# Kernel tuning notes

Hardware: AMD Instinct MI355X
Metric: run time of the kernel (lower is better)

The kernel has to match this reference:

```python
import jax, jax.numpy as jnp
import numpy as np

N_HEADS = 16
D_MODEL = 512
HEAD_DIM = D_MODEL // N_HEADS
SCALE = 1.0 / (HEAD_DIM ** 0.5)
R = 4  # LSREF radius -> window = step = 2*r = 8


def _layernorm(x, g, b, eps=1e-5):
    m = x.mean(axis=-1, keepdims=True)
    v = x.var(axis=-1, keepdims=True)
    return (x - m) / jnp.sqrt(v + eps) * g + b


def _mha(q_in, k_in, v_in, wq, bq, wk, bk, wv, bv, wo, bo):
    # Informer FullAttention(mask_flag=False), AttentionLayer(mix=False), eval mode (no dropout)
    B, L, _ = q_in.shape
    S = k_in.shape[1]
    q = (q_in @ wq.T + bq).reshape(B, L, N_HEADS, HEAD_DIM)
    k = (k_in @ wk.T + bk).reshape(B, S, N_HEADS, HEAD_DIM)
    v = (v_in @ wv.T + bv).reshape(B, S, N_HEADS, HEAD_DIM)
    scores = jnp.einsum('blhe,bshe->bhls', q, k) * SCALE
    A = jax.nn.softmax(scores, axis=-1)
    out = jnp.einsum('bhls,bshd->blhd', A, v).reshape(B, L, D_MODEL)
    return out @ wo.T + bo


def setup_inputs() -> dict:
    key = jax.random.key(0)
    ks = jax.random.split(key, 32)
    B, L, C, GL, DFF = 4, 1024, 512, 4096, 2048

    def w(k, shape, s=0.02):
        return (jax.random.normal(k, shape, jnp.float32) * s).astype(jnp.float32)

    inp = {
        'x': jax.random.normal(ks[0], (B, L, C), jnp.float32),
        'global_feat': jax.random.normal(ks[1], (B, C, GL), jnp.float32),
        'conv_w': w(ks[2], (C, C)), 'conv_b': jnp.zeros((C,), jnp.float32),
        'sa_wq': w(ks[3], (C, C)), 'sa_bq': jnp.zeros((C,), jnp.float32),
        'sa_wk': w(ks[4], (C, C)), 'sa_bk': jnp.zeros((C,), jnp.float32),
        'sa_wv': w(ks[5], (C, C)), 'sa_bv': jnp.zeros((C,), jnp.float32),
        'sa_wo': w(ks[6], (C, C)), 'sa_bo': jnp.zeros((C,), jnp.float32),
        'ca_wq': w(ks[7], (C, C)), 'ca_bq': jnp.zeros((C,), jnp.float32),
        'ca_wk': w(ks[8], (C, C)), 'ca_bk': jnp.zeros((C,), jnp.float32),
        'ca_wv': w(ks[9], (C, C)), 'ca_bv': jnp.zeros((C,), jnp.float32),
        'ca_wo': w(ks[10], (C, C)), 'ca_bo': jnp.zeros((C,), jnp.float32),
        'ffn_w1': w(ks[11], (DFF, C)), 'ffn_b1': jnp.zeros((DFF,), jnp.float32),
        'ffn_w2': w(ks[12], (C, DFF)), 'ffn_b2': jnp.zeros((C,), jnp.float32),
        'n1_g': jnp.ones((C,), jnp.float32), 'n1_b': jnp.zeros((C,), jnp.float32),
        'n2_g': jnp.ones((C,), jnp.float32), 'n2_b': jnp.zeros((C,), jnp.float32),
        'n3_g': jnp.ones((C,), jnp.float32), 'n3_b': jnp.zeros((C,), jnp.float32),
    }
    return inp


def reference(x, global_feat, conv_w, conv_b,
              sa_wq, sa_bq, sa_wk, sa_bk, sa_wv, sa_bv, sa_wo, sa_bo,
              ca_wq, ca_bq, ca_wk, ca_bk, ca_wv, ca_bv, ca_wo, ca_bo,
              ffn_w1, ffn_b1, ffn_w2, ffn_b2,
              n1_g, n1_b, n2_g, n2_b, n3_g, n3_b):
    # --- sliding_window_gaussian: non-overlapping windows (step == window == 2r) ---
    B, C, GL = global_feat.shape
    win_sz = 2 * R
    nw = (GL - win_sz) // win_sz + 1
    win = global_feat[:, :, :nw * win_sz].reshape(B, C, nw, win_sz)
    # torch.norm over a keepdim=1 axis is just |max - min|
    res = jnp.abs(win.max(axis=-1) - win.min(axis=-1)) + 1e-6  # [B, C, nw]
    # conv1d kernel size 1 == channelwise linear, then relu
    res = jax.nn.relu(jnp.einsum('oc,bcn->bon', conv_w, res) + conv_b[None, :, None])
    cross = res  # [B, 512, nw=512] consumed as [B, S, d_model]

    # --- CrossPyramidFusion: one Informer-style layer (self-attn, cross-attn, conv FFN) ---
    h = x + _mha(x, x, x, sa_wq, sa_bq, sa_wk, sa_bk, sa_wv, sa_bv, sa_wo, sa_bo)
    h = _layernorm(h, n1_g, n1_b)
    h = h + _mha(h, cross, cross, ca_wq, ca_bq, ca_wk, ca_bk, ca_wv, ca_bv, ca_wo, ca_bo)
    h = _layernorm(h, n2_g, n2_b)
    y = jax.nn.gelu(h @ ffn_w1.T + ffn_b1, approximate=False)
    y = y @ ffn_w2.T + ffn_b2
    out = _layernorm(h + y, n3_g, n3_b)
    return out.transpose(0, 2, 1)  # [B, 512, L]
```

## Files before the change

kernel.cpp:

```cpp
#include <hip/hip_runtime.h>
#include <hip/hip_bf16.h>
#include <math.h>

#define SCALE_Q 0.25504522f

typedef unsigned short u16;
typedef unsigned int u32;
typedef __attribute__((ext_vector_type(8))) short bshort8;
typedef __attribute__((ext_vector_type(4))) short sshort4;
typedef __attribute__((ext_vector_type(4))) float f32x4;
typedef __attribute__((ext_vector_type(4))) u32 u32x4;

__device__ inline u16 f2b(float f) {
    union { float f; uint32_t u; } c;
    c.f = f;
    uint32_t u = c.u;
    return (u16)((u + 0x7fffu + ((u >> 16) & 1u)) >> 16);
}

__device__ __forceinline__ u32 cvtpk(float a, float b) {
    u32 r;
    asm("v_cvt_pk_bf16_f32 %0, %1, %2" : "=v"(r) : "v"(a), "v"(b));
    return r;
}

__device__ __forceinline__ float exp2c(float s) {
    float c = fminf(s, 100.f);
    float r;
    asm("v_exp_f32 %0, %1" : "=v"(r) : "v"(c));
    return r;
}

__device__ inline void gload_lds16(const void* g, void* lds) {
    __builtin_amdgcn_global_load_lds(
        (const __attribute__((address_space(1))) void*)g,
        (__attribute__((address_space(3))) void*)lds, 16, 0, 0);
}

struct WSrc { const float* p[12]; };
__global__ __launch_bounds__(256) void wconv_kernel(WSrc s, u16* __restrict__ dst) {
    long e = ((long)blockIdx.x * 256 + threadIdx.x) * 4;
    if (e >= 6553600) return;
    int w; long base;
    if (e < 2359296)      { w = (int)(e >> 18); base = (long)w << 18; }
    else if (e < 3407872) { w = 9;  base = 2359296; }
    else if (e < 4456448) { w = 10; base = 3407872; }
    else                  { w = 11; base = 4456448; }
    float4 v = *(const float4*)(s.p[w] + (e - base));
    dst[e + 0] = f2b(v.x); dst[e + 1] = f2b(v.y);
    dst[e + 2] = f2b(v.z); dst[e + 3] = f2b(v.w);
}

__global__ __launch_bounds__(256) void win_kernel(const float* __restrict__ G,
                                                  u16* __restrict__ Rt, int total) {
    int i = blockIdx.x * 256 + threadIdx.x;
    if (i >= total) return;
    const float4* p = reinterpret_cast<const float4*>(G) + (size_t)i * 2;
    float4 a = p[0], b = p[1];
    float mx = fmaxf(fmaxf(fmaxf(a.x, a.y), fmaxf(a.z, a.w)),
                     fmaxf(fmaxf(b.x, b.y), fmaxf(b.z, b.w)));
    float mn = fminf(fminf(fminf(a.x, a.y), fminf(a.z, a.w)),
                     fminf(fminf(b.x, b.y), fminf(b.z, b.w)));
    int b_ = i >> 18, c = (i >> 9) & 511, n = i & 511;
    Rt[((long)(b_ * 512 + n) << 9) + c] = f2b(fabsf(mx - mn) + 1e-6f);
}

template <int BIASMODE, int ACT, bool RESID, int OUTMODE>
__device__ __forceinline__ void gemm_epilogue_elem(
    float v, int row, int col, int N, long zoff,
    const float* bias, const float* Rres, void* Cout,
    u16* D1, u16* D2, const float* bias1, const float* bias2) {
    if (OUTMODE == 3) {
        int grp = col >> 9, c = col & 511;
        float bb = (grp == 0) ? bias[c] : (grp == 1) ? bias1[c] : bias2[c];
        float vv = v + bb;
        if (grp == 0)
            ((u16*)Cout)[(long)row * 512 + c] = f2b(vv * SCALE_Q);
        else if (grp == 1)
            D1[(long)row * 512 + c] = f2b(vv);
        else
            D2[((long)((row >> 10) * 512 + c) << 10) + (row & 1023)] = f2b(vv);
    } else if (OUTMODE == 4) {
        int grp = col >> 9, c = col & 511;
        float vv = v + ((grp == 0) ? bias[c] : bias1[c]);
        if (grp == 0)
            ((u16*)Cout)[(long)row * 512 + c] = f2b(vv);
        else
            D2[((long)((row >> 9) * 512 + c) << 9) + (row & 511)] = f2b(vv);
    } else {
        if (BIASMODE == 1) v += bias[col];
        if (BIASMODE == 2) v += bias[row];
        if (ACT == 1) v = fmaxf(v, 0.f);
        if (ACT == 2) v = 0.5f * v * (1.f + erff(v * 0.70710678118654752f));
        if (ACT == 3) v *= SCALE_Q;
        if (RESID) v += Rres[(long)row * N + col];
        long off = zoff + (long)row * N + col;
        if (OUTMODE == 1) ((u16*)Cout)[off] = f2b(v);
        else              ((float*)Cout)[off] = v;
    }
}

template <int BIASMODE, int ACT, bool RESID, int OUTMODE>
__global__ __launch_bounds__(256) void bgemm64_kernel(
    const u16* __restrict__ A, const u16* __restrict__ Bt,
    const float* __restrict__ bias, const float* __restrict__ Rres,
    void* __restrict__ Cout, int M, int N, int K,
    long sA, long sB, long sC,
    u16* __restrict__ D1, u16* __restrict__ D2,
    const float* __restrict__ bias1, const float* __restrict__ bias2) {
    A  += (long)blockIdx.z * sA;
    Bt += (long)blockIdx.z * sB;
    __shared__ u16 As[2][64 * 64];
    __shared__ u16 Bs[2][64 * 64];
    int tid = threadIdx.x;
    int lane = tid & 63, wv = tid >> 6;
    int wr = wv >> 1, wc = wv & 1;
    int m0 = blockIdx.x * 64, n0 = blockIdx.y * 64;
    f32x4 acc[2][2] = {};
    int srow = lane >> 3;
    int selem = ((lane & 7) ^ srow) << 3;

    auto STAGE = [&](int buf, int k0) {
        #pragma unroll
        for (int i = 0; i < 2; i++) {
            int roff = i * 32 + wv * 8;
            gload_lds16(A + (long)(m0 + roff + srow) * K + k0 + selem,
                        (char*)As[buf] + roff * 128);
            gload_lds16(Bt + (long)(n0 + roff + srow) * K + k0 + selem,
                        (char*)Bs[buf] + roff * 128);
        }
    };

    int NT = K >> 6;
    STAGE(0, 0);
    int cur = 0;
    for (int kt = 0; kt < NT; ++kt) {
        if (kt + 1 < NT) {
            STAGE(cur ^ 1, (kt + 1) << 6);
            asm volatile("s_waitcnt vmcnt(4)\ns_barrier" ::: "memory");
        } else {
            asm volatile("s_waitcnt vmcnt(0)\ns_barrier" ::: "memory");
        }
        #pragma unroll
        for (int ks = 0; ks < 2; ks++) {
            bshort8 af[2], bf[2];
            int kbo = ks * 64 + ((lane >> 4) << 4);
            #pragma unroll
            for (int f = 0; f < 2; f++) {
                int arow = wr * 32 + f * 16 + (lane & 15);
                af[f] = *(const bshort8*)((const char*)As[cur] + arow * 128 +
                                          (kbo ^ ((arow & 7) << 4)));
                int brow = wc * 32 + f * 16 + (lane & 15);
                bf[f] = *(const bshort8*)((const char*)Bs[cur] + brow * 128 +
                                          (kbo ^ ((brow & 7) << 4)));
            }
            #pragma unroll
            for (int fi = 0; fi < 2; fi++)
                #pragma unroll
                for (int fj = 0; fj < 2; fj++)
                    acc[fi][fj] = __builtin_amdgcn_mfma_f32_16x16x32_bf16(
                        af[fi], bf[fj], acc[fi][fj], 0, 0, 0);
        }
        asm volatile("s_barrier" ::: "memory");
        cur ^= 1;
    }
    long zoff = (long)blockIdx.z * sC;
    #pragma unroll
    for (int fi = 0; fi < 2; fi++)
        #pragma unroll
        for (int fj = 0; fj < 2; fj++)
            #pragma unroll
            for (int r = 0; r < 4; r++) {
                int row = m0 + wr * 32 + fi * 16 + ((lane >> 4) << 2) + r;
                int col = n0 + wc * 32 + fj * 16 + (lane & 15);
                gemm_epilogue_elem<BIASMODE, ACT, RESID, OUTMODE>(
                    acc[fi][fj][r], row, col, N, zoff, bias, Rres, Cout,
                    D1, D2, bias1, bias2);
            }
}

__global__ __launch_bounds__(512) void attn_mfma_kernel(
    const u16* __restrict__ Q, const u16* __restrict__ K,
    const u16* __restrict__ Vt, u16* __restrict__ O, int L, int S) {
    __shared__ __align__(16) u16 Ks[2][2048];
    __shared__ __align__(16) u16 Vs[2][2048];
    int bh = blockIdx.x;
    int b = bh >> 4, h = bh & 15;
    int tid = threadIdx.x;
    int lane = tid & 63, wv = tid >> 6;
    int q0 = blockIdx.y * 128 + wv * 16;
    int qr = lane & 15, g = lane >> 4, g8 = g * 8;
    int kperm = 8 * (qr >> 2) + (qr & 3);
    int nt = S >> 6;

    const u16* Kb = K + (long)b * S * 512 + h * 32;
    const u16* Vb = Vt + ((long)b * 512 + h * 32) * S;
    bshort8 qf = *(const bshort8*)(Q + ((long)(b * L + q0 + qr)) * 512 + h * 32 + g8);

    const u16* src;
    long step;
    char *d0, *d1;
    if (wv < 4) {
        int rk = wv * 16 + (lane >> 2);
        int f = ((rk >> 3) & 3) ^ ((rk >> 1) & 3);
        int sc = (lane & 3) ^ f;
        src = Kb + (long)rk * 512 + sc * 8;
        step = (long)64 * 512;
        d0 = (char*)Ks[0] + wv * 1024;
        d1 = (char*)Ks[1] + wv * 1024;
    } else {
        int rv = (wv - 4) * 8 + (lane >> 3);
        int sc = (lane & 7) ^ (lane >> 3);
        src = Vb + (long)rv * S + sc * 8;
        step = 64;
        d0 = (char*)Vs[0] + (wv - 4) * 1024;
        d1 = (char*)Vs[1] + (wv - 4) * 1024;
    }

    f32x4 acc0 = {}, acc1 = {};
    float lsum = 0.f;
    int f0 = (qr >> 2) ^ ((qr >> 1) & 1);
    int f1 = f0 ^ 2;

    gload_lds16(src, d0);
    int cur = 0;
    for (int t = 0; t < nt; ++t) {
        if (t + 1 < nt) {
            gload_lds16(src + (long)(t + 1) * step, cur ? d0 : d1);
            asm volatile("s_waitcnt vmcnt(1)\ns_barrier" ::: "memory");
        } else {
            asm volatile("s_waitcnt vmcnt(0)\ns_barrier" ::: "memory");
        }
        const char* Kt = (const char*)Ks[cur];
        const char* Vl = (const char*)Vs[cur];
        bshort8 a0 = *(const bshort8*)(Kt + kperm * 64 + ((g ^ f0) << 4));
        bshort8 a1 = *(const bshort8*)(Kt + (kperm + 4) * 64 + ((g ^ f1) << 4));
        bshort8 a2 = *(const bshort8*)(Kt + (kperm + 32) * 64 + ((g ^ f0) << 4));
        bshort8 a3 = *(const bshort8*)(Kt + (kperm + 36) * 64 + ((g ^ f1) << 4));
        bshort8 v00 = *(const bshort8*)(Vl + qr * 128 + ((g ^ (qr & 7)) << 4));
        bshort8 v01 = *(const bshort8*)(Vl + qr * 128 + (((g + 4) ^ (qr & 7)) << 4));
        bshort8 v10 = *(const bshort8*)(Vl + (16 + qr) * 128 + ((g ^ (qr & 7)) << 4));
        bshort8 v11 = *(const bshort8*)(Vl + (16 + qr) * 128 + (((g + 4) ^ (qr & 7)) << 4));
        f32x4 zz = {0.f, 0.f, 0.f, 0.f};
        f32x4 st0 = __builtin_amdgcn_mfma_f32_16x16x32_bf16(a0, qf, zz, 0, 0, 0);
        f32x4 st1 = __builtin_amdgcn_mfma_f32_16x16x32_bf16(a1, qf, zz, 0, 0, 0);
        f32x4 st2 = __builtin_amdgcn_mfma_f32_16x16x32_bf16(a2, qf, zz, 0, 0, 0);
        f32x4 st3 = __builtin_amdgcn_mfma_f32_16x16x32_bf16(a3, qf, zz, 0, 0, 0);
        float p0[4], p1[4], p2[4], p3[4];
        #pragma unroll
        for (int r = 0; r < 4; r++) {
            p0[r] = exp2c(st0[r]);
            p1[r] = exp2c(st1[r]);
            p2[r] = exp2c(st2[r]);
            p3[r] = exp2c(st3[r]);
        }
        float ps = ((p0[0] + p0[1]) + (p0[2] + p0[3])) + ((p1[0] + p1[1]) + (p1[2] + p1[3])) +
                   ((p2[0] + p2[1]) + (p2[2] + p2[3])) + ((p3[0] + p3[1]) + (p3[2] + p3[3]));
        lsum += ps;
        u32x4 P0 = { cvtpk(p0[0], p0[1]), cvtpk(p0[2], p0[3]),
                     cvtpk(p1[0], p1[1]), cvtpk(p1[2], p1[3]) };
        u32x4 P1 = { cvtpk(p2[0], p2[1]), cvtpk(p2[2], p2[3]),
                     cvtpk(p3[0], p3[1]), cvtpk(p3[2], p3[3]) };
        bshort8 pf0 = *(bshort8*)&P0;
        bshort8 pf1 = *(bshort8*)&P1;
        acc0 = __builtin_amdgcn_mfma_f32_16x16x32_bf16(v00, pf0, acc0, 0, 0, 0);
        acc0 = __builtin_amdgcn_mfma_f32_16x16x32_bf16(v01, pf1, acc0, 0, 0, 0);
        acc1 = __builtin_amdgcn_mfma_f32_16x16x32_bf16(v10, pf0, acc1, 0, 0, 0);
        acc1 = __builtin_amdgcn_mfma_f32_16x16x32_bf16(v11, pf1, acc1, 0, 0, 0);
        asm volatile("s_barrier" ::: "memory");
        cur ^= 1;
    }

    lsum += __shfl_xor(lsum, 16);
    lsum += __shfl_xor(lsum, 32);
    float inv = 1.f / lsum;
    u16* op = O + ((long)(b * L + q0 + qr)) * 512 + h * 32 + g * 4;
    sshort4 o0, o1;
    #pragma unroll
    for (int r = 0; r < 4; r++) {
        o0[r] = (short)f2b(acc0[r] * inv);
        o1[r] = (short)f2b(acc1[r] * inv);
    }
    *(sshort4*)op = o0;
    *(sshort4*)(op + 16) = o1;
}

__global__ __launch_bounds__(256) void ln_kernel(const float* __restrict__ X,
                                                 const float* __restrict__ g,
                                                 const float* __restrict__ bt,
                                                 float* __restrict__ Y,
                                                 u16* __restrict__ Yb) {
    int row = blockIdx.x;
    const float* xr = X + (long)row * 512;
    int t = threadIdx.x;
    float x0 = xr[t], x1 = xr[t + 256];
    float s = x0 + x1, ss = x0 * x0 + x1 * x1;
    #pragma unroll
    for (int off = 32; off > 0; off >>= 1) {
        s += __shfl_down(s, off);
        ss += __shfl_down(ss, off);
    }
    __shared__ float sred[4], ssred[4];
    int wid = t >> 6;
    if ((t & 63) == 0) { sred[wid] = s; ssred[wid] = ss; }
    __syncthreads();
    float ts = sred[0] + sred[1] + sred[2] + sred[3];
    float tss = ssred[0] + ssred[1] + ssred[2] + ssred[3];
    float mean = ts * (1.f / 512.f);
    float var = tss * (1.f / 512.f) - mean * mean;
    float rstd = rsqrtf(var + 1e-5f);
    float y0 = (x0 - mean) * rstd * g[t] + bt[t];
    float y1 = (x1 - mean) * rstd * g[t + 256] + bt[t + 256];
    Y[(long)row * 512 + t] = y0;
    Y[(long)row * 512 + t + 256] = y1;
    Yb[(long)row * 512 + t] = f2b(y0);
    Yb[(long)row * 512 + t + 256] = f2b(y1);
}

__global__ __launch_bounds__(256) void ln_stats_kernel(const float* __restrict__ X,
                                                       float2* __restrict__ stats) {
    int row = blockIdx.x * 4 + (threadIdx.x >> 6);
    int lane = threadIdx.x & 63;
    const float4* xr = (const float4*)(X + (long)row * 512) + lane * 2;
    float4 a = xr[0], b = xr[1];
    float s = (a.x + a.y) + (a.z + a.w) + (b.x + b.y) + (b.z + b.w);
    float ss = (a.x * a.x + a.y * a.y) + (a.z * a.z + a.w * a.w) +
               (b.x * b.x + b.y * b.y) + (b.z * b.z + b.w * b.w);
    #pragma unroll
    for (int off = 32; off > 0; off >>= 1) {
        s += __shfl_down(s, off);
        ss += __shfl_down(ss, off);
    }
    if (lane == 0) {
        float mean = s * (1.f / 512.f);
        float var = ss * (1.f / 512.f) - mean * mean;
        stats[row] = make_float2(mean, rsqrtf(var + 1e-5f));
    }
}

__global__ __launch_bounds__(256) void ln_trans_kernel(
    const float* __restrict__ X, const float2* __restrict__ stats,
    const float* __restrict__ g, const float* __restrict__ bt,
    float* __restrict__ Y) {
    __shared__ float T[64][65];
    int b = blockIdx.z, l0 = blockIdx.x * 64, c0 = blockIdx.y * 64;
    int t = threadIdx.x;
    int col = t & 63, rq = t >> 6;
    #pragma unroll
    for (int i = 0; i < 16; i++) {
        int row = i * 4 + rq;
        T[row][col] = X[((long)(b * 1024 + l0 + row)) * 512 + c0 + col];
    }
    __syncthreads();
    float2 mr = stats[b * 1024 + l0 + col];
    #pragma unroll
    for (int i = 0; i < 16; i++) {
        int c = i * 4 + rq;
        float val = (T[col][c] - mr.x) * mr.y * g[c0 + c] + bt[c0 + c];
        Y[((long)(b * 512 + c0 + c)) * 1024 + l0 + col] = val;
    }
}

extern "C" void kernel_launch(void* const* d_in, const int* in_sizes, int n_in,
                              void* d_out, int out_size, void* d_ws, size_t ws_size,
                              hipStream_t stream) {
    const float* x      = (const float*)d_in[0];
    const float* gfeat  = (const float*)d_in[1];
    const float* conv_w = (const float*)d_in[2];
    const float* conv_b = (const float*)d_in[3];
    const float* sa_wq = (const float*)d_in[4];
    const float* sa_bq = (const float*)d_in[5];
    const float* sa_wk = (const float*)d_in[6];
    const float* sa_bk = (const float*)d_in[7];
    const float* sa_wv = (const float*)d_in[8];
    const float* sa_bv = (const float*)d_in[9];
    const float* sa_wo = (const float*)d_in[10];
    const float* sa_bo = (const float*)d_in[11];
    const float* ca_wq = (const float*)d_in[12];
    const float* ca_bq = (const float*)d_in[13];
    const float* ca_wk = (const float*)d_in[14];
    const float* ca_bk = (const float*)d_in[15];
    const float* ca_wv = (const float*)d_in[16];
    const float* ca_bv = (const float*)d_in[17];
    const float* ca_wo = (const float*)d_in[18];
    const float* ca_bo = (const float*)d_in[19];
    const float* ffn_w1 = (const float*)d_in[20];
    const float* ffn_b1 = (const float*)d_in[21];
    const float* ffn_w2 = (const float*)d_in[22];
    const float* ffn_b2 = (const float*)d_in[23];
    const float* n1_g = (const float*)d_in[24];
    const float* n1_b = (const float*)d_in[25];
    const float* n2_g = (const float*)d_in[26];
    const float* n2_b = (const float*)d_in[27];
    const float* n3_g = (const float*)d_in[28];
    const float* n3_b = (const float*)d_in[29];
    (void)ws_size; (void)n_in; (void)in_sizes; (void)out_size;

    const long M_ = 1048576;
    float* W0 = (float*)d_ws;
    float* h   = W0;
    float* hn  = W0 + 2 * M_;
    u16* U = (u16*)(W0 + 4 * M_);
    u16* qb     = U;
    u16* kb     = U + 2 * M_;
    u16* vtb    = U + 4 * M_;
    u16* k2b    = U + 6 * M_;
    u16* v2tb   = U + 7 * M_;
    u16* attb   = U + 8 * M_;
    u16* hnb    = U + 10 * M_;
    u16* midb   = U + 12 * M_;
    u16* wsb    = U + 20 * M_;
    u16* res_tb = U + 27 * M_;
    u16* crossb = U + 28 * M_;

    float2* ln3_stats = (float2*)res_tb;

    const u16* conv_wb = wsb;
    const u16* sa_wqb = wsb + 262144;
    const u16* sa_wob = wsb + 1048576;
    const u16* ca_wqb = wsb + 1310720;
    const u16* ca_wkb = wsb + 1572864;
    const u16* ca_wob = wsb + 2097152;
    const u16* ffn1b = wsb + 2359296, *ffn2b = wsb + 3407872;
    const u16* xb = wsb + 4456448;

    WSrc ws;
    ws.p[0] = conv_w; ws.p[1] = sa_wq; ws.p[2] = sa_wk; ws.p[3] = sa_wv;
    ws.p[4] = sa_wo; ws.p[5] = ca_wq; ws.p[6] = ca_wk; ws.p[7] = ca_wv;
    ws.p[8] = ca_wo; ws.p[9] = ffn_w1; ws.p[10] = ffn_w2; ws.p[11] = x;
    wconv_kernel<<<6400, 256, 0, stream>>>(ws, wsb);

    win_kernel<<<4096, 256, 0, stream>>>(gfeat, res_tb, 4 * 512 * 512);

    bgemm64_kernel<2, 1, false, 1><<<dim3(8, 8, 4), 256, 0, stream>>>(
        conv_wb, res_tb, conv_b, nullptr, crossb, 512, 512, 512, 0, 262144, 262144,
        nullptr, nullptr, nullptr, nullptr);

    bgemm64_kernel<1, 0, false, 3><<<dim3(64, 24), 256, 0, stream>>>(
        xb, sa_wqb, sa_bq, nullptr, qb, 4096, 1536, 512, 0, 0, 0,
        kb, vtb, sa_bk, sa_bv);

    attn_mfma_kernel<<<dim3(64, 8), 512, 0, stream>>>(qb, kb, vtb, attb, 1024, 1024);

    bgemm64_kernel<1, 0, true, 0><<<dim3(64, 8), 256, 0, stream>>>(
        attb, sa_wob, sa_bo, x, h, 4096, 512, 512, 0, 0, 0,
        nullptr, nullptr, nullptr, nullptr);

    ln_kernel<<<4096, 256, 0, stream>>>(h, n1_g, n1_b, hn, hnb);

    bgemm64_kernel<1, 3, false, 1><<<dim3(64, 8), 256, 0, stream>>>(
        hnb, ca_wqb, ca_bq, nullptr, qb, 4096, 512, 512, 0, 0, 0,
        nullptr, nullptr, nullptr, nullptr);
    bgemm64_kernel<1, 0, false, 4><<<dim3(32, 16), 256, 0, stream>>>(
        crossb, ca_wkb, ca_bk, nullptr, k2b, 2048, 1024, 512, 0, 0, 0,
        nullptr, v2tb, ca_bv, nullptr);

    attn_mfma_kernel<<<dim3(64, 8), 512, 0, stream>>>(qb, k2b, v2tb, attb, 1024, 512);

    bgemm64_kernel<1, 0, true, 0><<<dim3(64, 8), 256, 0, stream>>>(
        attb, ca_wob, ca_bo, hn, h, 4096, 512, 512, 0, 0, 0,
        nullptr, nullptr, nullptr, nullptr);

    ln_kernel<<<4096, 256, 0, stream>>>(h, n2_g, n2_b, hn, hnb);

    bgemm64_kernel<1, 2, false, 1><<<dim3(64, 32), 256, 0, stream>>>(
        hnb, ffn1b, ffn_b1, nullptr, midb, 4096, 2048, 512, 0, 0, 0,
        nullptr, nullptr, nullptr, nullptr);

    bgemm64_kernel<1, 0, true, 0><<<dim3(64, 8), 256, 0, stream>>>(
        midb, ffn2b, ffn_b2, hn, h, 4096, 512, 2048, 0, 0, 0,
        nullptr, nullptr, nullptr, nullptr);

    ln_stats_kernel<<<1024, 256, 0, stream>>>(h, ln3_stats);
    ln_trans_kernel<<<dim3(16, 8, 4), 256, 0, stream>>>(
        h, ln3_stats, n3_g, n3_b, (float*)d_out);
}
```

Baseline: 173.9 us.

## Merge prep kernels with LDS-transposed window reduce; triple-buffer attention loads

```diff
diff --git a/kernel.cpp b/kernel.cpp
--- a/kernel.cpp
+++ b/kernel.cpp
@@ -38,31 +38,44 @@
 }
 
 struct WSrc { const float* p[12]; };
-__global__ __launch_bounds__(256) void wconv_kernel(WSrc s, u16* __restrict__ dst) {
-    long e = ((long)blockIdx.x * 256 + threadIdx.x) * 4;
-    if (e >= 6553600) return;
-    int w; long base;
-    if (e < 2359296)      { w = (int)(e >> 18); base = (long)w << 18; }
-    else if (e < 3407872) { w = 9;  base = 2359296; }
-    else if (e < 4456448) { w = 10; base = 3407872; }
-    else                  { w = 11; base = 4456448; }
-    float4 v = *(const float4*)(s.p[w] + (e - base));
-    dst[e + 0] = f2b(v.x); dst[e + 1] = f2b(v.y);
-    dst[e + 2] = f2b(v.z); dst[e + 3] = f2b(v.w);
-}
-
-__global__ __launch_bounds__(256) void win_kernel(const float* __restrict__ G,
-                                                  u16* __restrict__ Rt, int total) {
-    int i = blockIdx.x * 256 + threadIdx.x;
-    if (i >= total) return;
-    const float4* p = reinterpret_cast<const float4*>(G) + (size_t)i * 2;
-    float4 a = p[0], b = p[1];
-    float mx = fmaxf(fmaxf(fmaxf(a.x, a.y), fmaxf(a.z, a.w)),
-                     fmaxf(fmaxf(b.x, b.y), fmaxf(b.z, b.w)));
-    float mn = fminf(fminf(fminf(a.x, a.y), fminf(a.z, a.w)),
-                     fminf(fminf(b.x, b.y), fminf(b.z, b.w)));
-    int b_ = i >> 18, c = (i >> 9) & 511, n = i & 511;
-    Rt[((long)(b_ * 512 + n) << 9) + c] = f2b(fabsf(mx - mn) + 1e-6f);
+__global__ __launch_bounds__(256) void prep_kernel(WSrc s, u16* __restrict__ dst,
+                                                   const float* __restrict__ G,
+                                                   u16* __restrict__ Rt) {
+    int bid = blockIdx.x;
+    if (bid < 256) {
+        __shared__ u16 T[64][72];
+        int b = bid >> 6, c0 = ((bid >> 3) & 7) << 6, n0 = (bid & 7) << 6;
+        int t = threadIdx.x;
+        int n = t & 63, cq = t >> 6;
+        const float* Gb = G + (long)b * 512 * 4096;
+        #pragma unroll
+        for (int i = 0; i < 16; i++) {
+            int c = i * 4 + cq;
+            const float4* p = (const float4*)(Gb + (long)(c0 + c) * 4096 + (n0 + n) * 8);
+            float4 a = p[0], bb = p[1];
+            float mx = fmaxf(fmaxf(fmaxf(a.x, a.y), fmaxf(a.z, a.w)),
+                             fmaxf(fmaxf(bb.x, bb.y), fmaxf(bb.z, bb.w)));
+            float mn = fminf(fminf(fminf(a.x, a.y), fminf(a.z, a.w)),
+                             fminf(fminf(bb.x, bb.y), fminf(bb.z, bb.w)));
+            T[n][c] = f2b(fabsf(mx - mn) + 1e-6f);
+        }
+        __syncthreads();
+        int nr = t >> 2, ck = (t & 3) << 4;
+        u16* o = Rt + ((long)(b * 512 + n0 + nr) << 9) + c0 + ck;
+        *(bshort8*)o = *(const bshort8*)&T[nr][ck];
+        *(bshort8*)(o + 8) = *(const bshort8*)&T[nr][ck + 8];
+    } else {
+        long e = ((long)(bid - 256) * 256 + threadIdx.x) * 4;
+        if (e >= 6553600) return;
+        int w; long base;
+        if (e < 2359296)      { w = (int)(e >> 18); base = (long)w << 18; }
+        else if (e < 3407872) { w = 9;  base = 2359296; }
+        else if (e < 4456448) { w = 10; base = 3407872; }
+        else                  { w = 11; base = 4456448; }
+        float4 v = *(const float4*)(s.p[w] + (e - base));
+        dst[e + 0] = f2b(v.x); dst[e + 1] = f2b(v.y);
+        dst[e + 2] = f2b(v.z); dst[e + 3] = f2b(v.w);
+    }
 }
 
 template <int BIASMODE, int ACT, bool RESID, int OUTMODE>
@@ -182,8 +195,8 @@
 __global__ __launch_bounds__(512) void attn_mfma_kernel(
     const u16* __restrict__ Q, const u16* __restrict__ K,
     const u16* __restrict__ Vt, u16* __restrict__ O, int L, int S) {
-    __shared__ __align__(16) u16 Ks[2][2048];
-    __shared__ __align__(16) u16 Vs[2][2048];
+    __shared__ __align__(16) u16 Ks[3][2048];
+    __shared__ __align__(16) u16 Vs[3][2048];
     int bh = blockIdx.x;
     int b = bh >> 4, h = bh & 15;
     int tid = threadIdx.x;
@@ -199,7 +212,7 @@
 
     const u16* src;
     long step;
-    char *d0, *d1;
+    char* d0;
     if (wv < 4) {
         int rk = wv * 16 + (lane >> 2);
         int f = ((rk >> 3) & 3) ^ ((rk >> 1) & 3);
@@ -207,32 +220,35 @@
         src = Kb + (long)rk * 512 + sc * 8;
         step = (long)64 * 512;
         d0 = (char*)Ks[0] + wv * 1024;
-        d1 = (char*)Ks[1] + wv * 1024;
     } else {
         int rv = (wv - 4) * 8 + (lane >> 3);
         int sc = (lane & 7) ^ (lane >> 3);
         src = Vb + (long)rv * S + sc * 8;
         step = 64;
         d0 = (char*)Vs[0] + (wv - 4) * 1024;
-        d1 = (char*)Vs[1] + (wv - 4) * 1024;
-    }
-
-    f32x4 acc0 = {}, acc1 = {};
-    float lsum = 0.f;
+    }
+
+    f32x4 acc0 = {}, acc1 = {}, acc2 = {};
+    const bshort8 onesf = { (short)0x3F80, (short)0x3F80, (short)0x3F80, (short)0x3F80,
+                            (short)0x3F80, (short)0x3F80, (short)0x3F80, (short)0x3F80 };
     int f0 = (qr >> 2) ^ ((qr >> 1) & 1);
     int f1 = f0 ^ 2;
 
     gload_lds16(src, d0);
+    gload_lds16(src + step, d0 + 4096);
     int cur = 0;
     for (int t = 0; t < nt; ++t) {
-        if (t + 1 < nt) {
-            gload_lds16(src + (long)(t + 1) * step, cur ? d0 : d1);
+        if (t + 2 < nt) {
+            int nb = cur + 2; if (nb >= 3) nb -= 3;
+            gload_lds16(src + (long)(t + 2) * step, d0 + nb * 4096);
+            asm volatile("s_waitcnt vmcnt(2)\ns_barrier" ::: "memory");
+        } else if (t + 1 < nt) {
             asm volatile("s_waitcnt vmcnt(1)\ns_barrier" ::: "memory");
         } else {
             asm volatile("s_waitcnt vmcnt(0)\ns_barrier" ::: "memory");
         }
-        const char* Kt = (const char*)Ks[cur];
-        const char* Vl = (const char*)Vs[cur];
+        const char* Kt = (const char*)Ks[0] + cur * 4096;
+        const char* Vl = (const char*)Vs[0] + cur * 4096;
         bshort8 a0 = *(const bshort8*)(Kt + kperm * 64 + ((g ^ f0) << 4));
         bshort8 a1 = *(const bshort8*)(Kt + (kperm + 4) * 64 + ((g ^ f1) << 4));
         bshort8 a2 = *(const bshort8*)(Kt + (kperm + 32) * 64 + ((g ^ f0) << 4));
@@ -254,9 +270,6 @@
             p2[r] = exp2c(st2[r]);
             p3[r] = exp2c(st3[r]);
         }
-        float ps = ((p0[0] + p0[1]) + (p0[2] + p0[3])) + ((p1[0] + p1[1]) + (p1[2] + p1[3])) +
-                   ((p2[0] + p2[1]) + (p2[2] + p2[3])) + ((p3[0] + p3[1]) + (p3[2] + p3[3]));
-        lsum += ps;
         u32x4 P0 = { cvtpk(p0[0], p0[1]), cvtpk(p0[2], p0[3]),
                      cvtpk(p1[0], p1[1]), cvtpk(p1[2], p1[3]) };
         u32x4 P1 = { cvtpk(p2[0], p2[1]), cvtpk(p2[2], p2[3]),
@@ -267,13 +280,13 @@
         acc0 = __builtin_amdgcn_mfma_f32_16x16x32_bf16(v01, pf1, acc0, 0, 0, 0);
         acc1 = __builtin_amdgcn_mfma_f32_16x16x32_bf16(v10, pf0, acc1, 0, 0, 0);
         acc1 = __builtin_amdgcn_mfma_f32_16x16x32_bf16(v11, pf1, acc1, 0, 0, 0);
+        acc2 = __builtin_amdgcn_mfma_f32_16x16x32_bf16(onesf, pf0, acc2, 0, 0, 0);
+        acc2 = __builtin_amdgcn_mfma_f32_16x16x32_bf16(onesf, pf1, acc2, 0, 0, 0);
         asm volatile("s_barrier" ::: "memory");
-        cur ^= 1;
-    }
-
-    lsum += __shfl_xor(lsum, 16);
-    lsum += __shfl_xor(lsum, 32);
-    float inv = 1.f / lsum;
+        cur = (cur == 2) ? 0 : cur + 1;
+    }
+
+    float inv = 1.f / acc2[0];
     u16* op = O + ((long)(b * L + q0 + qr)) * 512 + h * 32 + g * 4;
     sshort4 o0, o1;
     #pragma unroll
@@ -428,9 +441,7 @@
     ws.p[0] = conv_w; ws.p[1] = sa_wq; ws.p[2] = sa_wk; ws.p[3] = sa_wv;
     ws.p[4] = sa_wo; ws.p[5] = ca_wq; ws.p[6] = ca_wk; ws.p[7] = ca_wv;
     ws.p[8] = ca_wo; ws.p[9] = ffn_w1; ws.p[10] = ffn_w2; ws.p[11] = x;
-    wconv_kernel<<<6400, 256, 0, stream>>>(ws, wsb);
-
-    win_kernel<<<4096, 256, 0, stream>>>(gfeat, res_tb, 4 * 512 * 512);
+    prep_kernel<<<6656, 256, 0, stream>>>(ws, wsb, gfeat, res_tb);
 
     bgemm64_kernel<2, 1, false, 1><<<dim3(8, 8, 4), 256, 0, stream>>>(
         conv_wb, res_tb, conv_b, nullptr, crossb, 512, 512, 512, 0, 262144, 262144,
```

Result: faster. 168.2 us (-3.3%).
